# Kernel optimization log

Hardware: AMD Instinct MI355X
Metric: run time of the kernel (lower is better)

The kernel has to match this reference:

```python
import jax, jax.numpy as jnp
import numpy as np

EPS = 1e-5  # torch LayerNorm default

def layernorm(x, g, b):
    mu = jnp.mean(x, axis=-1, keepdims=True)
    var = jnp.mean(jnp.square(x - mu), axis=-1, keepdims=True)
    return (x - mu) * jax.lax.rsqrt(var + EPS) * g + b

def setup_inputs() -> dict:
    key = jax.random.key(0)
    ks = jax.random.split(key, 12)
    B, L1, L2 = 8, 2048, 2048
    D1, D2, E = 1024, 768, 1024
    s1, s2, se = D1 ** -0.5, D2 ** -0.5, E ** -0.5
    return {
        "modality1": jax.random.normal(ks[0], (B, L1, D1), jnp.float32),
        "modality2": jax.random.normal(ks[1], (B, L2, D2), jnp.float32),
        "ln1_g": jnp.ones((D1,), jnp.float32),
        "ln1_b": jnp.zeros((D1,), jnp.float32),
        "ln2_g": jnp.ones((D2,), jnp.float32),
        "ln2_b": jnp.zeros((D2,), jnp.float32),
        "Wq": jax.random.normal(ks[2], (D1, E), jnp.float32) * s1,
        "bq": jax.random.normal(ks[3], (E,), jnp.float32) * 0.01,
        "Wk": jax.random.normal(ks[4], (D2, E), jnp.float32) * s2,
        "bk": jax.random.normal(ks[5], (E,), jnp.float32) * 0.01,
        "Wv": jax.random.normal(ks[6], (D2, E), jnp.float32) * s2,
        "bv": jax.random.normal(ks[7], (E,), jnp.float32) * 0.01,
        "Wo": jax.random.normal(ks[8], (E, D1), jnp.float32) * se,
        "bo": jax.random.normal(ks[9], (D1,), jnp.float32) * 0.01,
    }

def reference(modality1, modality2, ln1_g, ln1_b, ln2_g, ln2_b,
              Wq, bq, Wk, bk, Wv, bv, Wo, bo):
    E = Wq.shape[1]
    scaling = E ** -0.5
    x1 = layernorm(modality1, ln1_g, ln1_b)   # [B, L1, D1]
    x2 = layernorm(modality2, ln2_g, ln2_b)   # [B, L2, D2]
    q = x1 @ Wq + bq                           # [B, L1, E]
    k = x2 @ Wk + bk                           # [B, L2, E]
    v = x2 @ Wv + bv                           # [B, L2, E]
    scores = jnp.einsum('bqe,bke->bqk', q, k) * scaling
    attn = jax.nn.softmax(scores, axis=-1)     # [B, L1, L2]
    ctx = jnp.einsum('bqk,bke->bqe', attn, v)  # [B, L1, E]
    return ctx @ Wo + bo                        # [B, L1, D1]
```

## Files before the change

kernel.cpp:

```cpp
#include <hip/hip_runtime.h>
#include <hip/hip_bf16.h>

typedef __bf16 bf16_t;
typedef __bf16 bf16x4_t __attribute__((ext_vector_type(4)));
typedef __bf16 bf16x8_t __attribute__((ext_vector_type(8)));
typedef float f32x4_t __attribute__((ext_vector_type(4)));
typedef float f32x16_t __attribute__((ext_vector_type(16)));

typedef __attribute__((address_space(1))) void gvoid_t;
typedef __attribute__((address_space(3))) void svoid_t;

__device__ __forceinline__ void gload_lds16(const void* g, void* s) {
    __builtin_amdgcn_global_load_lds((gvoid_t*)g, (svoid_t*)s, 16, 0, 0);
}

template <typename CT, bool BIAS, bool STORE_T = false>
__global__ __launch_bounds__(256, 2)
void gemm_bt(const bf16_t* __restrict__ A, const bf16_t* __restrict__ Bt,
             CT* __restrict__ C, const float* __restrict__ bias,
             int M, int N, int K, float scale,
             size_t sA, size_t sB, size_t sC, int tshift)
{
    __shared__ bf16_t As[128 * 32];
    __shared__ bf16_t Bs[128 * 32];

    const int nx = gridDim.x, ny = gridDim.y;
    const int nblk = nx * ny * (int)gridDim.z;
    int lin = blockIdx.x + nx * (blockIdx.y + ny * blockIdx.z);
    int tile = lin;
    if ((nblk & 7) == 0)
        tile = (lin & 7) * (nblk >> 3) + (lin >> 3);
    const int per_z = nx * ny;
    const int bz = tile / per_z;
    int t = tile - bz * per_z;
    const int SB = 8;
    const int band = t / (nx * SB);
    const int r = t - band * (nx * SB);
    const int h = min(SB, ny - band * SB);
    const int bx = r / h;
    const int by = band * SB + (r - bx * h);

    A  += (size_t)bz * sA;
    Bt += (size_t)bz * sB;
    C  += (size_t)bz * sC;

    const int tid  = threadIdx.x;
    const int wave = tid >> 6;
    const int lane = tid & 63;
    const int m0 = by * 128;
    const int n0 = bx * 128;

    const int c0 = tid, c1 = tid + 256;
    const int r0 = c0 >> 2, r1 = c1 >> 2;
    const int k0c = (((c0 & 3) ^ ((r0 >> 1) & 3))) * 8;
    const int k1c = (((c1 & 3) ^ ((r1 >> 1) & 3))) * 8;
    const bf16_t* ag0 = A  + (size_t)(m0 + r0) * K + k0c;
    const bf16_t* ag1 = A  + (size_t)(m0 + r1) * K + k1c;
    const bf16_t* bg0 = Bt + (size_t)(n0 + r0) * K + k0c;
    const bf16_t* bg1 = Bt + (size_t)(n0 + r1) * K + k1c;
    bf16_t* asb0 = As + (size_t)(wave * 64) * 8;
    bf16_t* asb1 = As + (size_t)(wave * 64 + 256) * 8;
    bf16_t* bsb0 = Bs + (size_t)(wave * 64) * 8;
    bf16_t* bsb1 = Bs + (size_t)(wave * 64 + 256) * 8;

    const int lr  = lane & 31;
    const int kh  = lane >> 5;
    const int swz = (lr >> 1) & 3;
    const int wm = (wave >> 1) * 64;
    const int wn = (wave & 1) * 64;

    f32x16_t acc[2][2];
#pragma unroll
    for (int i = 0; i < 2; ++i)
#pragma unroll
        for (int j = 0; j < 2; ++j)
            acc[i][j] = (f32x16_t)(0.f);

    for (int kt = 0; kt < K; kt += 32) {
        gload_lds16(ag0, asb0);
        gload_lds16(ag1, asb1);
        gload_lds16(bg0, bsb0);
        gload_lds16(bg1, bsb1);
        ag0 += 32; ag1 += 32; bg0 += 32; bg1 += 32;
        __builtin_amdgcn_s_waitcnt(0);
        __syncthreads();

        bf16x8_t af[2][2], bfr[2][2];
#pragma unroll
        for (int mi = 0; mi < 2; ++mi)
#pragma unroll
            for (int kk = 0; kk < 2; ++kk)
                af[mi][kk] = *(const bf16x8_t*)
                    &As[(wm + mi * 32 + lr) * 32 + ((2 * kk + kh) ^ swz) * 8];
#pragma unroll
        for (int nj = 0; nj < 2; ++nj)
#pragma unroll
            for (int kk = 0; kk < 2; ++kk)
                bfr[nj][kk] = *(const bf16x8_t*)
                    &Bs[(wn + nj * 32 + lr) * 32 + ((2 * kk + kh) ^ swz) * 8];
#pragma unroll
        for (int mi = 0; mi < 2; ++mi)
#pragma unroll
            for (int nj = 0; nj < 2; ++nj)
#pragma unroll
                for (int kk = 0; kk < 2; ++kk)
                    acc[mi][nj] = __builtin_amdgcn_mfma_f32_32x32x16_bf16(
                        af[mi][kk], bfr[nj][kk], acc[mi][nj], 0, 0, 0);
        __syncthreads();
    }

#pragma unroll
    for (int nj = 0; nj < 2; ++nj) {
        const int col = n0 + wn + nj * 32 + lr;
        const float bv = BIAS ? bias[col] : 0.0f;
#pragma unroll
        for (int mi = 0; mi < 2; ++mi) {
            f32x16_t v = acc[mi][nj];
#pragma unroll
            for (int g = 0; g < 4; ++g) {
                const int row = m0 + wm + mi * 32 + 8 * g + 4 * kh;
                if constexpr (STORE_T) {
                    const int b = row >> tshift;
                    const int l = row & ((1 << tshift) - 1);
                    bf16x4_t o;
#pragma unroll
                    for (int rr = 0; rr < 4; ++rr)
                        o[rr] = (bf16_t)(v[g * 4 + rr] * scale + bv);
                    *(bf16x4_t*)((bf16_t*)C + ((size_t)b * N << tshift) +
                                 ((size_t)col << tshift) + l) = o;
                } else {
#pragma unroll
                    for (int rr = 0; rr < 4; ++rr) {
                        float val = v[g * 4 + rr] * scale + bv;
                        C[(size_t)(row + rr) * N + col] = (CT)val;
                    }
                }
            }
        }
    }
}

template <int NV>
__global__ __launch_bounds__(256, 4)
void layernorm_k(const float* __restrict__ x, const float* __restrict__ g,
                 const float* __restrict__ b, bf16_t* __restrict__ y)
{
    const int D = NV * 256;
    const int wave = threadIdx.x >> 6, lane = threadIdx.x & 63;
    const size_t row = (size_t)blockIdx.x * 4 + wave;
    const float4* xr = (const float4*)(x + row * D);

    float4 v[NV];
    float s = 0.f, sq = 0.f;
#pragma unroll
    for (int i = 0; i < NV; ++i) {
        v[i] = xr[lane + 64 * i];
        s  += v[i].x + v[i].y + v[i].z + v[i].w;
        sq += v[i].x * v[i].x + v[i].y * v[i].y + v[i].z * v[i].z + v[i].w * v[i].w;
    }
#pragma unroll
    for (int m = 32; m; m >>= 1) {
        s  += __shfl_xor(s, m, 64);
        sq += __shfl_xor(sq, m, 64);
    }
    const float mean = s / D;
    const float rstd = rsqrtf(fmaxf(sq / D - mean * mean, 0.f) + 1e-5f);

#pragma unroll
    for (int i = 0; i < NV; ++i) {
        const int c4 = lane + 64 * i;
        float4 gg = ((const float4*)g)[c4];
        float4 bb = ((const float4*)b)[c4];
        bf16x4_t o;
        o[0] = (bf16_t)((v[i].x - mean) * rstd * gg.x + bb.x);
        o[1] = (bf16_t)((v[i].y - mean) * rstd * gg.y + bb.y);
        o[2] = (bf16_t)((v[i].z - mean) * rstd * gg.z + bb.z);
        o[3] = (bf16_t)((v[i].w - mean) * rstd * gg.w + bb.w);
        *(bf16x4_t*)(y + row * D + (size_t)c4 * 4) = o;
    }
}

__global__ __launch_bounds__(256, 4)
void softmax_rows(bf16_t* __restrict__ a)
{
    const int wave = threadIdx.x >> 6, lane = threadIdx.x & 63;
    const size_t row = (size_t)blockIdx.x * 4 + wave;
    bf16_t* r = a + row * 2048;

    float v[32];
    float mx = -3.0e38f;
#pragma unroll
    for (int i = 0; i < 4; ++i) {
        bf16x8_t t = *(const bf16x8_t*)(r + (size_t)(lane + 64 * i) * 8);
#pragma unroll
        for (int j = 0; j < 8; ++j) {
            v[i * 8 + j] = (float)t[j];
            mx = fmaxf(mx, v[i * 8 + j]);
        }
    }
#pragma unroll
    for (int m = 32; m; m >>= 1) mx = fmaxf(mx, __shfl_xor(mx, m, 64));
    float s = 0.f;
#pragma unroll
    for (int i = 0; i < 32; ++i) { v[i] = __expf(v[i] - mx); s += v[i]; }
#pragma unroll
    for (int m = 32; m; m >>= 1) s += __shfl_xor(s, m, 64);
    const float rs = 1.0f / s;
#pragma unroll
    for (int i = 0; i < 4; ++i) {
        bf16x8_t t;
#pragma unroll
        for (int j = 0; j < 8; ++j) t[j] = (bf16_t)(v[i * 8 + j] * rs);
        *(bf16x8_t*)(r + (size_t)(lane + 64 * i) * 8) = t;
    }
}

__global__ __launch_bounds__(256, 4)
void wconvT(const float* __restrict__ w, bf16_t* __restrict__ wt, int K, int N)
{
    __shared__ float s[32][33];
    const int tx = threadIdx.x, ty = threadIdx.y;
    const int n0 = blockIdx.x * 32, k0 = blockIdx.y * 32;
#pragma unroll
    for (int r = 0; r < 4; ++r)
        s[ty + r * 8][tx] = w[(size_t)(k0 + ty + r * 8) * N + n0 + tx];
    __syncthreads();
#pragma unroll
    for (int r = 0; r < 4; ++r)
        wt[(size_t)(n0 + ty + r * 8) * K + k0 + tx] = (bf16_t)s[tx][ty + r * 8];
}


extern "C" void kernel_launch(void* const* d_in, const int* in_sizes, int n_in,
                              void* d_out, int out_size, void* d_ws, size_t ws_size,
                              hipStream_t stream)
{
    const int B = 8, L1 = 2048, L2 = 2048, D1 = 1024, D2 = 768, E = 1024;
    const float scale = 0.03125f;
    const int tsh = 11;

    const float* m1   = (const float*)d_in[0];
    const float* m2   = (const float*)d_in[1];
    const float* ln1g = (const float*)d_in[2];
    const float* ln1b = (const float*)d_in[3];
    const float* ln2g = (const float*)d_in[4];
    const float* ln2b = (const float*)d_in[5];
    const float* Wq   = (const float*)d_in[6];
    const float* bq   = (const float*)d_in[7];
    const float* Wk   = (const float*)d_in[8];
    const float* bk   = (const float*)d_in[9];
    const float* Wv   = (const float*)d_in[10];
    const float* bv   = (const float*)d_in[11];
    const float* Wo   = (const float*)d_in[12];
    const float* bo   = (const float*)d_in[13];
    float* out = (float*)d_out;

    bf16_t* ws = (bf16_t*)d_ws;
    size_t off = 0;
    auto alloc = [&](size_t n) { bf16_t* p = ws + off; off += n; return p; };
    bf16_t* WqT = alloc((size_t)E * D1);
    bf16_t* WkT = alloc((size_t)E * D2);
    bf16_t* WvT = alloc((size_t)E * D2);
    bf16_t* WoT = alloc((size_t)D1 * E);
    bf16_t* x1  = alloc((size_t)B * L1 * D1);
    bf16_t* x2  = alloc((size_t)B * L2 * D2);
    bf16_t* Qb  = alloc((size_t)B * L1 * E);
    bf16_t* Kb  = alloc((size_t)B * L2 * E);
    bf16_t* VTb = alloc((size_t)B * E * L2);
    bf16_t* ctx = alloc((size_t)B * L1 * E);
    bf16_t* attn = ws + off;
    const bool batched = (off + (size_t)B * L1 * L2) * sizeof(bf16_t) <= ws_size;

    dim3 blk256(256);

    wconvT<<<dim3(E / 32, D1 / 32), dim3(32, 8), 0, stream>>>(Wq, WqT, D1, E);
    wconvT<<<dim3(E / 32, D2 / 32), dim3(32, 8), 0, stream>>>(Wk, WkT, D2, E);
    wconvT<<<dim3(E / 32, D2 / 32), dim3(32, 8), 0, stream>>>(Wv, WvT, D2, E);
    wconvT<<<dim3(D1 / 32, E / 32), dim3(32, 8), 0, stream>>>(Wo, WoT, E, D1);

    layernorm_k<4><<<dim3(B * L1 / 4), blk256, 0, stream>>>(m1, ln1g, ln1b, x1);
    layernorm_k<3><<<dim3(B * L2 / 4), blk256, 0, stream>>>(m2, ln2g, ln2b, x2);

    gemm_bt<bf16_t, true><<<dim3(E / 128, B * L1 / 128, 1), blk256, 0, stream>>>(
        x1, WqT, Qb, bq, B * L1, E, D1, 1.0f, 0, 0, 0, 0);
    gemm_bt<bf16_t, true><<<dim3(E / 128, B * L2 / 128, 1), blk256, 0, stream>>>(
        x2, WkT, Kb, bk, B * L2, E, D2, 1.0f, 0, 0, 0, 0);
    gemm_bt<bf16_t, true, true><<<dim3(E / 128, B * L2 / 128, 1), blk256, 0, stream>>>(
        x2, WvT, VTb, bv, B * L2, E, D2, 1.0f, 0, 0, 0, tsh);

    if (batched) {
        gemm_bt<bf16_t, false><<<dim3(L2 / 128, L1 / 128, B), blk256, 0, stream>>>(
            Qb, Kb, attn, nullptr, L1, L2, E, scale,
            (size_t)L1 * E, (size_t)L2 * E, (size_t)L1 * L2, 0);
        softmax_rows<<<dim3(B * L1 / 4), blk256, 0, stream>>>(attn);
        gemm_bt<bf16_t, false><<<dim3(E / 128, L1 / 128, B), blk256, 0, stream>>>(
            attn, VTb, ctx, nullptr, L1, E, L2, 1.0f,
            (size_t)L1 * L2, (size_t)E * L2, (size_t)L1 * E, 0);
    } else {
        for (int b = 0; b < B; ++b) {
            gemm_bt<bf16_t, false><<<dim3(L2 / 128, L1 / 128, 1), blk256, 0, stream>>>(
                Qb + (size_t)b * L1 * E, Kb + (size_t)b * L2 * E, attn, nullptr,
                L1, L2, E, scale, 0, 0, 0, 0);
            softmax_rows<<<dim3(L1 / 4), blk256, 0, stream>>>(attn);
            gemm_bt<bf16_t, false><<<dim3(E / 128, L1 / 128, 1), blk256, 0, stream>>>(
                attn, VTb + (size_t)b * E * L2, ctx + (size_t)b * L1 * E, nullptr,
                L1, E, L2, 1.0f, 0, 0, 0, 0);
        }
    }

    gemm_bt<float, true><<<dim3(D1 / 128, B * L1 / 128, 1), blk256, 0, stream>>>(
        ctx, WoT, out, bo, B * L1, D1, E, 1.0f, 0, 0, 0, 0);
}
```

Measured before the change: 547.4 us.

## Use 256x256 tiles, 512 threads and a 4-stage LDS pipeline in GEMM

Rewrites the shared bf16 GEMM to compute 256x256 output tiles with 8 waves per block. It also adds a four-deep ring of LDS buffers filled by async global-to-LDS loads, with explicit vmcnt waits so loads overlap the MFMA work. MFMA sections run at raised wave priority. The aim is to improve data reuse and hide global memory latency, at the cost of 128KB of LDS per block, which limits occupancy to about one block per CU. It also yields fewer blocks for the small projection GEMMs, which may hurt load balance.

After: 573.1 us. +4.7%, slower.

```diff
diff --git a/kernel.cpp b/kernel.cpp
--- a/kernel.cpp
+++ b/kernel.cpp
@@ -14,15 +14,21 @@
     __builtin_amdgcn_global_load_lds((gvoid_t*)g, (svoid_t*)s, 16, 0, 0);
 }
 
+__device__ __forceinline__ void wg_barrier() {
+    asm volatile("" ::: "memory");
+    __builtin_amdgcn_s_barrier();
+    asm volatile("" ::: "memory");
+}
+
 template <typename CT, bool BIAS, bool STORE_T = false>
-__global__ __launch_bounds__(256, 2)
+__global__ __launch_bounds__(512, 2)
 void gemm_bt(const bf16_t* __restrict__ A, const bf16_t* __restrict__ Bt,
              CT* __restrict__ C, const float* __restrict__ bias,
              int M, int N, int K, float scale,
              size_t sA, size_t sB, size_t sC, int tshift)
 {
-    __shared__ bf16_t As[128 * 32];
-    __shared__ bf16_t Bs[128 * 32];
+    __shared__ bf16_t As[4 * 256 * 32];
+    __shared__ bf16_t Bs[4 * 256 * 32];
 
     const int nx = gridDim.x, ny = gridDim.y;
     const int nblk = nx * ny * (int)gridDim.z;
@@ -47,92 +53,116 @@
     const int tid  = threadIdx.x;
     const int wave = tid >> 6;
     const int lane = tid & 63;
-    const int m0 = by * 128;
-    const int n0 = bx * 128;
-
-    const int c0 = tid, c1 = tid + 256;
-    const int r0 = c0 >> 2, r1 = c1 >> 2;
-    const int k0c = (((c0 & 3) ^ ((r0 >> 1) & 3))) * 8;
-    const int k1c = (((c1 & 3) ^ ((r1 >> 1) & 3))) * 8;
-    const bf16_t* ag0 = A  + (size_t)(m0 + r0) * K + k0c;
-    const bf16_t* ag1 = A  + (size_t)(m0 + r1) * K + k1c;
-    const bf16_t* bg0 = Bt + (size_t)(n0 + r0) * K + k0c;
-    const bf16_t* bg1 = Bt + (size_t)(n0 + r1) * K + k1c;
-    bf16_t* asb0 = As + (size_t)(wave * 64) * 8;
-    bf16_t* asb1 = As + (size_t)(wave * 64 + 256) * 8;
-    bf16_t* bsb0 = Bs + (size_t)(wave * 64) * 8;
-    bf16_t* bsb1 = Bs + (size_t)(wave * 64 + 256) * 8;
-
-    const int lr  = lane & 31;
-    const int kh  = lane >> 5;
+    const int m0 = by * 256;
+    const int n0 = bx * 256;
+
+    const int rr = tid >> 2;
+    const int cc = ((tid & 3) ^ ((rr >> 1) & 3)) * 8;
+    const bf16_t* aw0 = A  + (size_t)(m0 + rr) * K + cc;
+    const bf16_t* aw1 = aw0 + (size_t)128 * K;
+    const bf16_t* bw0 = Bt + (size_t)(n0 + rr) * K + cc;
+    const bf16_t* bw1 = bw0 + (size_t)128 * K;
+    const int soff0 = wave * 512;
+    const int soff1 = 4096 + wave * 512;
+
+    const int wm = wave >> 2;
+    const int wn = wave & 3;
+    const int lr = lane & 31;
+    const int kh = lane >> 5;
     const int swz = (lr >> 1) & 3;
-    const int wm = (wave >> 1) * 64;
-    const int wn = (wave & 1) * 64;
-
-    f32x16_t acc[2][2];
-#pragma unroll
-    for (int i = 0; i < 2; ++i)
+
+    f32x16_t acc[4][2];
+#pragma unroll
+    for (int i = 0; i < 4; ++i)
 #pragma unroll
         for (int j = 0; j < 2; ++j)
             acc[i][j] = (f32x16_t)(0.f);
 
-    for (int kt = 0; kt < K; kt += 32) {
-        gload_lds16(ag0, asb0);
-        gload_lds16(ag1, asb1);
-        gload_lds16(bg0, bsb0);
-        gload_lds16(bg1, bsb1);
-        ag0 += 32; ag1 += 32; bg0 += 32; bg1 += 32;
-        __builtin_amdgcn_s_waitcnt(0);
-        __syncthreads();
-
-        bf16x8_t af[2][2], bfr[2][2];
-#pragma unroll
-        for (int mi = 0; mi < 2; ++mi)
+    const int NT = K >> 5;
+
+    auto stage = [&](int buf) {
+        bf16_t* a = As + buf * 8192;
+        bf16_t* b = Bs + buf * 8192;
+        gload_lds16(aw0, a + soff0);
+        gload_lds16(aw1, a + soff1);
+        gload_lds16(bw0, b + soff0);
+        gload_lds16(bw1, b + soff1);
+        aw0 += 32; aw1 += 32; bw0 += 32; bw1 += 32;
+    };
+
+    stage(0);
+    if (NT > 1) stage(1);
+    if (NT > 2) stage(2);
+
+    for (int j = 0; j < NT; ++j) {
+        const int buf = j & 3;
+        if (j + 3 < NT) {
+            stage((j + 3) & 3);
+            asm volatile("s_waitcnt vmcnt(12)" ::: "memory");
+        } else if (j + 2 < NT) {
+            asm volatile("s_waitcnt vmcnt(8)" ::: "memory");
+        } else if (j + 1 < NT) {
+            asm volatile("s_waitcnt vmcnt(4)" ::: "memory");
+        } else {
+            asm volatile("s_waitcnt vmcnt(0)" ::: "memory");
+        }
+        wg_barrier();
+
+        const bf16_t* ab = As + buf * 8192;
+        const bf16_t* bb = Bs + buf * 8192;
+        bf16x8_t af[4][2], bfr[2][2];
+#pragma unroll
+        for (int mi = 0; mi < 4; ++mi)
 #pragma unroll
             for (int kk = 0; kk < 2; ++kk)
                 af[mi][kk] = *(const bf16x8_t*)
-                    &As[(wm + mi * 32 + lr) * 32 + ((2 * kk + kh) ^ swz) * 8];
+                    &ab[(wm * 128 + mi * 32 + lr) * 32 + ((2 * kk + kh) ^ swz) * 8];
 #pragma unroll
         for (int nj = 0; nj < 2; ++nj)
 #pragma unroll
             for (int kk = 0; kk < 2; ++kk)
                 bfr[nj][kk] = *(const bf16x8_t*)
-                    &Bs[(wn + nj * 32 + lr) * 32 + ((2 * kk + kh) ^ swz) * 8];
-#pragma unroll
-        for (int mi = 0; mi < 2; ++mi)
-#pragma unroll
-            for (int nj = 0; nj < 2; ++nj)
-#pragma unroll
-                for (int kk = 0; kk < 2; ++kk)
+                    &bb[(wn * 64 + nj * 32 + lr) * 32 + ((2 * kk + kh) ^ swz) * 8];
+
+        __builtin_amdgcn_s_setprio(1);
+#pragma unroll
+        for (int kk = 0; kk < 2; ++kk)
+#pragma unroll
+            for (int mi = 0; mi < 4; ++mi)
+#pragma unroll
+                for (int nj = 0; nj < 2; ++nj)
                     acc[mi][nj] = __builtin_amdgcn_mfma_f32_32x32x16_bf16(
                         af[mi][kk], bfr[nj][kk], acc[mi][nj], 0, 0, 0);
-        __syncthreads();
+        __builtin_amdgcn_s_setprio(0);
+
+        asm volatile("s_waitcnt lgkmcnt(0)" ::: "memory");
+        wg_barrier();
     }
 
 #pragma unroll
     for (int nj = 0; nj < 2; ++nj) {
-        const int col = n0 + wn + nj * 32 + lr;
+        const int col = n0 + wn * 64 + nj * 32 + lr;
         const float bv = BIAS ? bias[col] : 0.0f;
 #pragma unroll
-        for (int mi = 0; mi < 2; ++mi) {
+        for (int mi = 0; mi < 4; ++mi) {
             f32x16_t v = acc[mi][nj];
 #pragma unroll
             for (int g = 0; g < 4; ++g) {
-                const int row = m0 + wm + mi * 32 + 8 * g + 4 * kh;
+                const int row = m0 + wm * 128 + mi * 32 + 8 * g + 4 * kh;
                 if constexpr (STORE_T) {
                     const int b = row >> tshift;
                     const int l = row & ((1 << tshift) - 1);
                     bf16x4_t o;
 #pragma unroll
-                    for (int rr = 0; rr < 4; ++rr)
-                        o[rr] = (bf16_t)(v[g * 4 + rr] * scale + bv);
+                    for (int rr2 = 0; rr2 < 4; ++rr2)
+                        o[rr2] = (bf16_t)(v[g * 4 + rr2] * scale + bv);
                     *(bf16x4_t*)((bf16_t*)C + ((size_t)b * N << tshift) +
                                  ((size_t)col << tshift) + l) = o;
                 } else {
 #pragma unroll
-                    for (int rr = 0; rr < 4; ++rr) {
-                        float val = v[g * 4 + rr] * scale + bv;
-                        C[(size_t)(row + rr) * N + col] = (CT)val;
+                    for (int rr2 = 0; rr2 < 4; ++rr2) {
+                        float val = v[g * 4 + rr2] * scale + bv;
+                        C[(size_t)(row + rr2) * N + col] = (CT)val;
                     }
                 }
             }
@@ -272,6 +302,7 @@
     const bool batched = (off + (size_t)B * L1 * L2) * sizeof(bf16_t) <= ws_size;
 
     dim3 blk256(256);
+    dim3 blk512(512);
 
     wconvT<<<dim3(E / 32, D1 / 32), dim3(32, 8), 0, stream>>>(Wq, WqT, D1, E);
     wconvT<<<dim3(E / 32, D2 / 32), dim3(32, 8), 0, stream>>>(Wk, WkT, D2, E);
@@ -281,33 +312,33 @@
     layernorm_k<4><<<dim3(B * L1 / 4), blk256, 0, stream>>>(m1, ln1g, ln1b, x1);
     layernorm_k<3><<<dim3(B * L2 / 4), blk256, 0, stream>>>(m2, ln2g, ln2b, x2);
 
-    gemm_bt<bf16_t, true><<<dim3(E / 128, B * L1 / 128, 1), blk256, 0, stream>>>(
+    gemm_bt<bf16_t, true><<<dim3(E / 256, B * L1 / 256, 1), blk512, 0, stream>>>(
         x1, WqT, Qb, bq, B * L1, E, D1, 1.0f, 0, 0, 0, 0);
-    gemm_bt<bf16_t, true><<<dim3(E / 128, B * L2 / 128, 1), blk256, 0, stream>>>(
+    gemm_bt<bf16_t, true><<<dim3(E / 256, B * L2 / 256, 1), blk512, 0, stream>>>(
         x2, WkT, Kb, bk, B * L2, E, D2, 1.0f, 0, 0, 0, 0);
-    gemm_bt<bf16_t, true, true><<<dim3(E / 128, B * L2 / 128, 1), blk256, 0, stream>>>(
+    gemm_bt<bf16_t, true, true><<<dim3(E / 256, B * L2 / 256, 1), blk512, 0, stream>>>(
         x2, WvT, VTb, bv, B * L2, E, D2, 1.0f, 0, 0, 0, tsh);
 
     if (batched) {
-        gemm_bt<bf16_t, false><<<dim3(L2 / 128, L1 / 128, B), blk256, 0, stream>>>(
+        gemm_bt<bf16_t, false><<<dim3(L2 / 256, L1 / 256, B), blk512, 0, stream>>>(
             Qb, Kb, attn, nullptr, L1, L2, E, scale,
             (size_t)L1 * E, (size_t)L2 * E, (size_t)L1 * L2, 0);
         softmax_rows<<<dim3(B * L1 / 4), blk256, 0, stream>>>(attn);
-        gemm_bt<bf16_t, false><<<dim3(E / 128, L1 / 128, B), blk256, 0, stream>>>(
+        gemm_bt<bf16_t, false><<<dim3(E / 256, L1 / 256, B), blk512, 0, stream>>>(
             attn, VTb, ctx, nullptr, L1, E, L2, 1.0f,
             (size_t)L1 * L2, (size_t)E * L2, (size_t)L1 * E, 0);
     } else {
         for (int b = 0; b < B; ++b) {
-            gemm_bt<bf16_t, false><<<dim3(L2 / 128, L1 / 128, 1), blk256, 0, stream>>>(
+            gemm_bt<bf16_t, false><<<dim3(L2 / 256, L1 / 256, 1), blk512, 0, stream>>>(
                 Qb + (size_t)b * L1 * E, Kb + (size_t)b * L2 * E, attn, nullptr,
                 L1, L2, E, scale, 0, 0, 0, 0);
             softmax_rows<<<dim3(L1 / 4), blk256, 0, stream>>>(attn);
-            gemm_bt<bf16_t, false><<<dim3(E / 128, L1 / 128, 1), blk256, 0, stream>>>(
+            gemm_bt<bf16_t, false><<<dim3(E / 256, L1 / 256, 1), blk512, 0, stream>>>(
                 attn, VTb + (size_t)b * E * L2, ctx + (size_t)b * L1 * E, nullptr,
                 L1, E, L2, 1.0f, 0, 0, 0, 0);
         }
     }
 
-    gemm_bt<float, true><<<dim3(D1 / 128, B * L1 / 128, 1), blk256, 0, stream>>>(
+    gemm_bt<float, true><<<dim3(D1 / 256, B * L1 / 256, 1), blk512, 0, stream>>>(
         ctx, WoT, out, bo, B * L1, D1, E, 1.0f, 0, 0, 0, 0);
 }
```
